# Performance work log

Measured on AMD Instinct MI355X. Metric: run time of the kernel, lower is better.

## Reference

```python
import jax, jax.numpy as jnp
import numpy as np

# ROIAlign config (torchvision semantics, aligned=False)
SPATIAL_SCALE = 0.25
POOLED = 7
SAMPLING_RATIO = 2
MODE = "max"  # from __init__ mode='max'


def setup_inputs() -> dict:
    key = jax.random.key(0)
    kf, kcx, kcy, kw, kh, kb = jax.random.split(key, 6)
    B, C, H, W = 2, 256, 200, 304
    N = 512
    IMG_H, IMG_W = H / SPATIAL_SCALE, W / SPATIAL_SCALE
    feature = jax.random.normal(kf, (B, C, H, W), dtype=jnp.float32)
    cx = jax.random.uniform(kcx, (N,)) * IMG_W
    cy = jax.random.uniform(kcy, (N,)) * IMG_H
    bw = jax.random.uniform(kw, (N,)) * 192.0 + 16.0
    bh = jax.random.uniform(kh, (N,)) * 192.0 + 16.0
    x1 = jnp.clip(cx - bw * 0.5, 0.0, IMG_W - 2.0)
    y1 = jnp.clip(cy - bh * 0.5, 0.0, IMG_H - 2.0)
    x2 = jnp.clip(cx + bw * 0.5, x1 + 1.0, IMG_W - 1.0)
    y2 = jnp.clip(cy + bh * 0.5, y1 + 1.0, IMG_H - 1.0)
    boxes = jnp.stack([x1, y1, x2, y2], axis=1).astype(jnp.float32)
    batch_idx = jax.random.randint(kb, (N,), 0, B, dtype=jnp.int32)
    return {"feature": feature, "boxes": boxes, "batch_idx": batch_idx}


def _sample_coords(start, size):
    # start,size: [N]; returns [N, POOLED*SAMPLING_RATIO] sample coordinates
    bin_sz = size / POOLED                         # [N]
    p = jnp.arange(POOLED, dtype=jnp.float32)      # bin index
    s = (jnp.arange(SAMPLING_RATIO, dtype=jnp.float32) + 0.5) / SAMPLING_RATIO
    # coord = start + (p + s) * bin_sz  -> [N, POOLED, RATIO]
    c = start[:, None, None] + (p[None, :, None] + s[None, None, :]) * bin_sz[:, None, None]
    return c.reshape(c.shape[0], POOLED * SAMPLING_RATIO)


def roi_align(feature, boxes, batch_idx):
    B, C, H, W = feature.shape
    roi = boxes * SPATIAL_SCALE                    # [N,4] in feature coords
    rs_x, rs_y, re_x, re_y = roi[:, 0], roi[:, 1], roi[:, 2], roi[:, 3]
    roi_w = jnp.maximum(re_x - rs_x, 1.0)
    roi_h = jnp.maximum(re_y - rs_y, 1.0)
    ys = _sample_coords(rs_y, roi_h)               # [N, Sy]
    xs = _sample_coords(rs_x, roi_w)               # [N, Sx]
    y = jnp.broadcast_to(ys[:, :, None], (ys.shape[0], ys.shape[1], xs.shape[1]))
    x = jnp.broadcast_to(xs[:, None, :], y.shape)  # [N, Sy, Sx]

    valid = (y > -1.0) & (y < H) & (x > -1.0) & (x < W)
    y = jnp.clip(y, 0.0, H - 1)
    x = jnp.clip(x, 0.0, W - 1)
    y0 = jnp.floor(y).astype(jnp.int32)
    x0 = jnp.floor(x).astype(jnp.int32)
    y1 = jnp.minimum(y0 + 1, H - 1)
    x1 = jnp.minimum(x0 + 1, W - 1)
    ly = y - y0.astype(y.dtype)
    lx = x - x0.astype(x.dtype)
    hy, hx = 1.0 - ly, 1.0 - lx
    b = batch_idx[:, None, None]
    # advanced indexing -> [N, Sy, Sx, C]
    val = (hy * hx)[..., None] * feature[b, :, y0, x0] \
        + (hy * lx)[..., None] * feature[b, :, y0, x1] \
        + (ly * hx)[..., None] * feature[b, :, y1, x0] \
        + (ly * lx)[..., None] * feature[b, :, y1, x1]
    val = jnp.where(valid[..., None], val, 0.0)
    N = boxes.shape[0]
    val = val.reshape(N, POOLED, SAMPLING_RATIO, POOLED, SAMPLING_RATIO, C)
    if MODE == "max":
        out = val.max(axis=(2, 4))                 # [N, PH, PW, C]
    else:
        out = val.mean(axis=(2, 4))
    return jnp.transpose(out, (0, 3, 1, 2))        # [N, C, PH, PW]


def reference(feature, boxes, batch_idx):
    return roi_align(feature, boxes, batch_idx)
```

## Files before the change

kernel.cpp:

```cpp
#include <hip/hip_runtime.h>


#define SPATIAL_SCALE 0.25f
#define POOLED 7
#define SR 2

constexpr int Cc = 256;
constexpr int Hc = 200;
constexpr int Wc = 304;
constexpr int Nc = 512;

constexpr int CG      = 4;
constexpr int TILES   = Cc / CG;
constexpr int NSAMP   = POOLED * SR;
constexpr int NROW    = NSAMP * 2;
constexpr int GRP     = 264;
constexpr int CH_F    = 7 * GRP;
constexpr int BUF_F   = CG * CH_F;
constexpr int CELLS   = POOLED * POOLED;
constexpr int PER_BOX = Cc * CELLS;
constexpr int PLANE   = Hc * Wc;

__global__ __launch_bounds__(256) void roi_align_max_kernel(
    const float* __restrict__ feature,
    const float* __restrict__ boxes,
    const int*   __restrict__ batch_idx,
    float*       __restrict__ out)
{
    __shared__ float lds[2 * BUF_F];

    const int n   = blockIdx.x;
    const int tid = threadIdx.x;
    const int wv     = tid >> 6;
    const int lane   = tid & 63;
    const int lane16 = lane & 15;
    const int rquad  = lane >> 4;

    const float rsx = boxes[n * 4 + 0] * SPATIAL_SCALE;
    const float rsy = boxes[n * 4 + 1] * SPATIAL_SCALE;
    const float rex = boxes[n * 4 + 2] * SPATIAL_SCALE;
    const float rey = boxes[n * 4 + 3] * SPATIAL_SCALE;
    const float roi_w = fmaxf(rex - rsx, 1.0f);
    const float roi_h = fmaxf(rey - rsy, 1.0f);
    const float bin_w = roi_w / (float)POOLED;
    const float bin_h = roi_h / (float)POOLED;
    const int   b     = batch_idx[n];

    const float x_first = __fadd_rn(rsx, __fmul_rn(0.25f, bin_w));
    const float xc0     = fminf(fmaxf(x_first, 0.0f), (float)(Wc - 1));
    const int   xbase   = ((int)floorf(xc0)) & ~3;

    const float x_last = __fadd_rn(rsx, __fmul_rn(6.75f, bin_w));
    const float xlc    = fminf(fmaxf(x_last, 0.0f), (float)(Wc - 1));
    const int   x0l    = (int)floorf(xlc);
    const int   xlastc = min(x0l + 1, Wc - 1);
    const int   span   = xlastc - xbase + 1;
    const int   nl4    = (span + 4) >> 2;

    int ro[7];
    #pragma unroll
    for (int it = 0; it < 7; ++it) {
        const int  slot  = it * 4 + rquad;
        const int  which = slot >= NSAMP;
        const int  sY    = which ? slot - NSAMP : slot;
        const float py   = fmaf((float)sY, 0.5f, 0.25f);
        const float fy   = __fadd_rn(rsy, __fmul_rn(py, bin_h));
        const float fyc  = fminf(fmaxf(fy, 0.0f), (float)(Hc - 1));
        const int   y0   = (int)floorf(fyc);
        const int   row  = which ? min(y0 + 1, Hc - 1) : y0;
        ro[it] = row * Wc;
    }
    const int  col = min(xbase + lane16 * 4, Wc - 4);
    const bool act = (lane16 < nl4);

    const int cell = min(lane, CELLS - 1);
    const int ph   = cell / POOLED;
    const int pw   = cell - ph * POOLED;

    float w00[2][2], w01[2][2], w10[2][2], w11[2][2];
    int   r0a[2][2], r1a[2][2];
    #pragma unroll
    for (int sy = 0; sy < SR; ++sy) {
        const int   sY  = ph * SR + sy;
        const float py  = (float)ph + ((float)sy + 0.5f) * 0.5f;
        const float fy  = __fadd_rn(rsy, __fmul_rn(py, bin_h));
        const bool  vy  = (fy > -1.0f) && (fy < (float)Hc);
        const float fyc = fminf(fmaxf(fy, 0.0f), (float)(Hc - 1));
        const int   y0i = (int)floorf(fyc);
        const float ly  = fyc - (float)y0i;
        const float hy  = 1.0f - ly;
        #pragma unroll
        for (int sx = 0; sx < SR; ++sx) {
            const float px  = (float)pw + ((float)sx + 0.5f) * 0.5f;
            const float fx  = __fadd_rn(rsx, __fmul_rn(px, bin_w));
            const bool  vx  = (fx > -1.0f) && (fx < (float)Wc);
            const float fxc = fminf(fmaxf(fx, 0.0f), (float)(Wc - 1));
            const int   x0i = (int)floorf(fxc);
            const float lx  = fxc - (float)x0i;
            const float hx  = 1.0f - lx;
            const int   c0  = x0i - xbase;
            const bool  v   = vy && vx;
            w00[sy][sx] = v ? hy * hx : 0.0f;
            w01[sy][sx] = v ? hy * lx : 0.0f;
            w10[sy][sx] = v ? ly * hx : 0.0f;
            w11[sy][sx] = v ? ly * lx : 0.0f;
            const int s0 = sY;
            const int s1 = NSAMP + sY;
            r0a[sy][sx] = (s0 >> 2) * GRP + (s0 & 3) * 64 + c0;
            r1a[sy][sx] = (s1 >> 2) * GRP + (s1 & 3) * 64 + c0;
        }
    }

    const float* __restrict__ gp0 =
        feature + ((size_t)b * Cc + wv) * (size_t)PLANE;

#define ISSUE_TILE(GT, Q)                                                     \
    if (act) {                                                                \
        _Pragma("unroll")                                                     \
        for (int it = 0; it < 7; ++it) {                                      \
            const float* gsrc = (GT) + ro[it] + col;                          \
            const int lofs = __builtin_amdgcn_readfirstlane(                  \
                ((Q) * BUF_F + wv * CH_F + it * GRP) * 4);                    \
            __builtin_amdgcn_global_load_lds(                                 \
                (const __attribute__((address_space(1))) unsigned int*)       \
                    (const void*)gsrc,                                        \
                (__attribute__((address_space(3))) unsigned int*)             \
                    (void*)((char*)lds + lofs),                               \
                16, 0, 0);                                                    \
        }                                                                     \
    }

    ISSUE_TILE(gp0, 0)
    const float* __restrict__ gnext = gp0 + (size_t)CG * PLANE;

    for (int j = 0; j < TILES; ++j) {
        if (j + 1 < TILES) {
            ISSUE_TILE(gnext, ((j + 1) & 1))
            gnext += (size_t)CG * PLANE;
            asm volatile("s_waitcnt vmcnt(7)" ::: "memory");
        } else {
            asm volatile("s_waitcnt vmcnt(0)" ::: "memory");
        }

        const int qb = (j & 1) * BUF_F + wv * CH_F;
        float m = -INFINITY;
        #pragma unroll
        for (int sy = 0; sy < SR; ++sy) {
            #pragma unroll
            for (int sx = 0; sx < SR; ++sx) {
                const int a0 = qb + r0a[sy][sx];
                const int a1 = qb + r1a[sy][sx];
                const float bil = w00[sy][sx] * lds[a0]
                                + w01[sy][sx] * lds[a0 + 1]
                                + w10[sy][sx] * lds[a1]
                                + w11[sy][sx] * lds[a1 + 1];
                m = fmaxf(m, bil);
            }
        }
        if (lane < CELLS)
            out[(size_t)n * PER_BOX + (size_t)(j * CG + wv) * CELLS + cell] = m;
    }
#undef ISSUE_TILE
}

extern "C" void kernel_launch(void* const* d_in, const int* in_sizes, int n_in,
                              void* d_out, int out_size, void* d_ws, size_t ws_size,
                              hipStream_t stream) {
    const float* feature   = (const float*)d_in[0];
    const float* boxes     = (const float*)d_in[1];
    const int*   batch_idx = (const int*)d_in[2];
    float*       out       = (float*)d_out;

    roi_align_max_kernel<<<Nc, 256, 0, stream>>>(feature, boxes,
                                                 batch_idx, out);
}
```

Baseline: 227.1 us.

## Sort boxes by batch and vertical band to improve per-XCD cache locality

Adds a small ranking kernel that sorts boxes by (batch index, vertical band of box center) and writes a permutation into the workspace. The main kernel maps block IDs through that permutation, and the (bid&7)*64+(bid>>3) mapping places boxes that are spatially close on the same XCD, so they share feature rows in that XCD's L2. The cost is an extra kernel launch and an extra indirect load per block. It also depends on a workspace being supplied.

```diff
diff --git a/kernel.cpp b/kernel.cpp
--- a/kernel.cpp
+++ b/kernel.cpp
@@ -21,15 +21,45 @@
 constexpr int PER_BOX = Cc * CELLS;
 constexpr int PLANE   = Hc * Wc;
 
+__global__ __launch_bounds__(64) void box_rank_kernel(
+    const float* __restrict__ boxes,
+    const int*   __restrict__ batch_idx,
+    int*         __restrict__ perm)
+{
+    const int n = blockIdx.x;
+    const int l = threadIdx.x;
+
+    const float cyn  = (boxes[n * 4 + 1] + boxes[n * 4 + 3])
+                     * (0.5f * SPATIAL_SCALE);
+    const int  bandn = min(3, max(0, (int)(cyn * (4.0f / (float)Hc))));
+    const int  keyn  = batch_idx[n] * 4 + bandn;
+
+    int rank = 0;
+    #pragma unroll
+    for (int m = 0; m < Nc / 64; ++m) {
+        const int j = m * 64 + l;
+        const float cyj  = (boxes[j * 4 + 1] + boxes[j * 4 + 3])
+                         * (0.5f * SPATIAL_SCALE);
+        const int  bandj = min(3, max(0, (int)(cyj * (4.0f / (float)Hc))));
+        const int  keyj  = batch_idx[j] * 4 + bandj;
+        const bool lt = (keyj < keyn) || (keyj == keyn && j < n);
+        rank += (int)__popcll(__ballot(lt));
+    }
+    if (l == 0) perm[rank] = n;
+}
+
+template <bool USE_PERM>
 __global__ __launch_bounds__(256) void roi_align_max_kernel(
     const float* __restrict__ feature,
     const float* __restrict__ boxes,
     const int*   __restrict__ batch_idx,
+    const int*   __restrict__ perm,
     float*       __restrict__ out)
 {
     __shared__ float lds[2 * BUF_F];
 
-    const int n   = blockIdx.x;
+    const int bid = blockIdx.x;
+    const int n = USE_PERM ? perm[(bid & 7) * 64 + (bid >> 3)] : bid;
     const int tid = threadIdx.x;
     const int wv     = tid >> 6;
     const int lane   = tid & 63;
@@ -171,6 +201,13 @@
     const int*   batch_idx = (const int*)d_in[2];
     float*       out       = (float*)d_out;
 
-    roi_align_max_kernel<<<Nc, 256, 0, stream>>>(feature, boxes,
-                                                 batch_idx, out);
+    if (d_ws != nullptr && ws_size >= (size_t)Nc * sizeof(int)) {
+        int* perm = (int*)d_ws;
+        box_rank_kernel<<<Nc, 64, 0, stream>>>(boxes, batch_idx, perm);
+        roi_align_max_kernel<true><<<Nc, 256, 0, stream>>>(
+            feature, boxes, batch_idx, perm, out);
+    } else {
+        roi_align_max_kernel<false><<<Nc, 256, 0, stream>>>(
+            feature, boxes, batch_idx, nullptr, out);
+    }
 }
```

Result: no change. 223.5 us (-1.5%).

## Stream feature planes per channel through an LDS row ring with sorted boxes

Applied to the files above, without the earlier changes.

Adds a prep kernel that sorts boxes by batch and top row and precomputes per-sample row and column interpolation tables into workspace. The main kernel is restructured so each block owns one (batch, channel) plane and streams its rows through a 64-row LDS ring. Groups of up to five boxes that fit in the window are processed together, so each feature row is read once per channel instead of once per box. This trades redundant global reads for an extra launch, serial box grouping and more barriers, and keeps the old per-box kernel as a fallback when workspace is missing.

```diff
diff --git a/kernel.cpp b/kernel.cpp
--- a/kernel.cpp
+++ b/kernel.cpp
@@ -1,166 +1,327 @@
 #include <hip/hip_runtime.h>
 
 
-#define SPATIAL_SCALE 0.25f
+#define SS 0.25f
 #define POOLED 7
-#define SR 2
 
 constexpr int Cc = 256;
 constexpr int Hc = 200;
 constexpr int Wc = 304;
 constexpr int Nc = 512;
 
-constexpr int CG      = 4;
-constexpr int TILES   = Cc / CG;
-constexpr int NSAMP   = POOLED * SR;
-constexpr int NROW    = NSAMP * 2;
-constexpr int GRP     = 264;
-constexpr int CH_F    = 7 * GRP;
-constexpr int BUF_F   = CG * CH_F;
-constexpr int CELLS   = POOLED * POOLED;
+constexpr int CELLS   = 49;
 constexpr int PER_BOX = Cc * CELLS;
 constexpr int PLANE   = Hc * Wc;
-
-__global__ __launch_bounds__(256) void roi_align_max_kernel(
-    const float* __restrict__ feature,
+constexpr int PLANE_B = PLANE * 4;
+constexpr int RING_ROWS = 64;
+constexpr int WIN     = 63;
+constexpr int RING_F  = RING_ROWS * Wc;
+constexpr int RING_B  = RING_F * 4;
+constexpr int RING_CH = RING_B / 1024;
+constexpr int G   = 5;
+constexpr int NS  = 14;
+
+constexpr int    TBL_OFF_B     = 2048;
+constexpr int    TBL_STRIDE_I4 = 28;
+constexpr size_t WS_NEED = TBL_OFF_B + (size_t)Nc * TBL_STRIDE_I4 * 16;
+
+__global__ __launch_bounds__(64) void roi_prep_kernel(
     const float* __restrict__ boxes,
     const int*   __restrict__ batch_idx,
+    unsigned int* __restrict__ meta,
+    int4*        __restrict__ tbl)
+{
+    const int n = blockIdx.x, l = threadIdx.x;
+
+    const float rsx = boxes[n*4+0]*SS, rsy = boxes[n*4+1]*SS;
+    const float rex = boxes[n*4+2]*SS, rey = boxes[n*4+3]*SS;
+    const float bin_h = fmaxf(rey - rsy, 1.0f) / (float)POOLED;
+    const float bin_w = fmaxf(rex - rsx, 1.0f) / (float)POOLED;
+    const int   batch = batch_idx[n];
+
+    const float fy0 = __fadd_rn(rsy, __fmul_rn(0.25f, bin_h));
+    const int y0min = (int)floorf(fminf(fmaxf(fy0, 0.f), (float)(Hc-1)));
+    const float fyL = __fadd_rn(rsy, __fmul_rn(6.75f, bin_h));
+    const int   yL  = (int)floorf(fminf(fmaxf(fyL, 0.f), (float)(Hc-1)));
+    const int ymax  = min(yL + 1, Hc - 1);
+    const unsigned key = (unsigned)(batch * 256 + y0min);
+
+    int rank = 0;
+    #pragma unroll
+    for (int m = 0; m < Nc/64; ++m) {
+        const int j = m*64 + l;
+        const float rsyj = boxes[j*4+1]*SS, reyj = boxes[j*4+3]*SS;
+        const float bhj  = fmaxf(reyj - rsyj, 1.0f) / (float)POOLED;
+        const float fyj  = __fadd_rn(rsyj, __fmul_rn(0.25f, bhj));
+        const int   yj   = (int)floorf(fminf(fmaxf(fyj,0.f),(float)(Hc-1)));
+        const unsigned keyj = (unsigned)(batch_idx[j]*256 + yj);
+        const bool lt = (keyj < key) || (keyj == key && j < n);
+        rank += (int)__popcll(__ballot(lt));
+    }
+    if (l == 0)
+        meta[rank] = (unsigned)n | ((unsigned)batch << 9)
+                   | ((unsigned)y0min << 10) | ((unsigned)ymax << 18);
+
+    if (l < NS) {
+        const float py  = fmaf((float)l, 0.5f, 0.25f);
+        const float fy  = __fadd_rn(rsy, __fmul_rn(py, bin_h));
+        const bool  vy  = (fy > -1.0f) && (fy < (float)Hc);
+        const float fyc = fminf(fmaxf(fy, 0.f), (float)(Hc-1));
+        const int   y0  = (int)floorf(fyc);
+        const float ly  = fyc - (float)y0, hy = 1.0f - ly;
+        int4 r; r.x = y0;
+        r.y = __float_as_int(vy ? hy : 0.0f);
+        r.z = __float_as_int(vy ? ly : 0.0f); r.w = 0;
+        tbl[n*TBL_STRIDE_I4 + l] = r;
+    } else if (l >= 16 && l < 16 + NS) {
+        const int s = l - 16;
+        const float px  = fmaf((float)s, 0.5f, 0.25f);
+        const float fx  = __fadd_rn(rsx, __fmul_rn(px, bin_w));
+        const bool  vx  = (fx > -1.0f) && (fx < (float)Wc);
+        const float fxc = fminf(fmaxf(fx, 0.f), (float)(Wc-1));
+        const int   x0  = (int)floorf(fxc);
+        const float lx  = fxc - (float)x0, hx = 1.0f - lx;
+        int4 r; r.x = x0;
+        r.y = __float_as_int(vx ? hx : 0.0f);
+        r.z = __float_as_int(vx ? lx : 0.0f); r.w = 0;
+        tbl[n*TBL_STRIDE_I4 + NS + s] = r;
+    }
+}
+
+__global__ __launch_bounds__(256) void roi_stream_kernel(
+    const float* __restrict__ feature,
+    const unsigned int* __restrict__ meta,
+    const int4*  __restrict__ tbl,
     float*       __restrict__ out)
 {
-    __shared__ float lds[2 * BUF_F];
-
-    const int n   = blockIdx.x;
-    const int tid = threadIdx.x;
-    const int wv     = tid >> 6;
-    const int lane   = tid & 63;
-    const int lane16 = lane & 15;
-    const int rquad  = lane >> 4;
-
-    const float rsx = boxes[n * 4 + 0] * SPATIAL_SCALE;
-    const float rsy = boxes[n * 4 + 1] * SPATIAL_SCALE;
-    const float rex = boxes[n * 4 + 2] * SPATIAL_SCALE;
-    const float rey = boxes[n * 4 + 3] * SPATIAL_SCALE;
-    const float roi_w = fmaxf(rex - rsx, 1.0f);
-    const float roi_h = fmaxf(rey - rsy, 1.0f);
-    const float bin_w = roi_w / (float)POOLED;
-    const float bin_h = roi_h / (float)POOLED;
-    const int   b     = batch_idx[n];
-
-    const float x_first = __fadd_rn(rsx, __fmul_rn(0.25f, bin_w));
-    const float xc0     = fminf(fmaxf(x_first, 0.0f), (float)(Wc - 1));
-    const int   xbase   = ((int)floorf(xc0)) & ~3;
-
-    const float x_last = __fadd_rn(rsx, __fmul_rn(6.75f, bin_w));
-    const float xlc    = fminf(fmaxf(x_last, 0.0f), (float)(Wc - 1));
-    const int   x0l    = (int)floorf(xlc);
-    const int   xlastc = min(x0l + 1, Wc - 1);
-    const int   span   = xlastc - xbase + 1;
-    const int   nl4    = (span + 4) >> 2;
+    __shared__ float ring[RING_F];
+
+    const int bid = blockIdx.x;
+    const int X = bid & 7, b = (bid >> 3) & 1, cj = bid >> 4;
+    const int c = X * 32 + cj;
+    const char* __restrict__ plane =
+        (const char*)(feature + ((size_t)b * Cc + c) * (size_t)PLANE);
+
+    const int tid = threadIdx.x, wv = tid >> 6, lane = tid & 63;
+    const int bg   = tid / CELLS;
+    const int cell = tid - bg * CELLS;
+    const int ph   = cell / POOLED, pw = cell - ph * POOLED;
+    const bool hasCell = (tid < G * CELLS);
+
+    int p = 0, loadedT = 0;
+
+    int cntA=0, yfA=0, tmA=0, nA0=0,nA1=0,nA2=0,nA3=0,nA4=0;
+    int cntB=0, yfB=0, tmB=0, nB0=0,nB1=0,nB2=0,nB3=0,nB4=0;
+    int4 ya0, ya1, xa0, xa1, yb0, yb1, xb0, xb1;
+
+#define COLLECT(CNT,YF,TM,N0,N1,N2,N3,N4) {                                  \
+    CNT = 0; YF = 0; TM = 0;                                                 \
+    while (p < Nc) {                                                         \
+        const unsigned mm = meta[p];                                         \
+        const int bt = (int)((mm >> 9) & 1u);                                \
+        if (bt != b) { if (bt < b) { ++p; continue; } else break; }          \
+        const int ymin = (int)((mm >> 10) & 255u);                           \
+        const int ymx  = (int)((mm >> 18) & 255u);                           \
+        const int nn   = (int)(mm & 511u);                                   \
+        if (CNT == 0) { YF = ymin; N0 = N1 = N2 = N3 = N4 = nn; }            \
+        else if (ymx + 1 > YF + WIN) break;                                  \
+        if      (CNT == 1) N1 = nn; else if (CNT == 2) N2 = nn;              \
+        else if (CNT == 3) N3 = nn; else if (CNT == 4) N4 = nn;              \
+        TM = max(TM, ymx + 1);                                               \
+        ++CNT; ++p;                                                          \
+        if (CNT == G) break;                                                 \
+    }                                                                        \
+}
+
+#define ISSUE(FROMT, TOT) {                                                  \
+    const int kc0 = (19*(FROMT) + 15) >> 4, kc1 = (19*(TOT) + 15) >> 4;      \
+    for (int k = kc0 + ((wv - kc0) & 3); k < kc1; k += 4) {                  \
+        const int km  = k % RING_CH;                                         \
+        const int off = k * 1024 + lane * 16;                                \
+        if (off < PLANE_B) {                                                 \
+            const int ldst = __builtin_amdgcn_readfirstlane(km * 1024);      \
+            __builtin_amdgcn_global_load_lds(                                \
+                (const __attribute__((address_space(1))) unsigned int*)      \
+                    (const void*)(plane + off),                              \
+                (__attribute__((address_space(3))) unsigned int*)            \
+                    (void*)((char*)ring + ldst), 16, 0, 0);                  \
+        }                                                                    \
+    }                                                                        \
+}
+
+#define LOADREC(N0,N1,N2,N3,N4, Y0,Y1,X0,X1) {                               \
+    const int nSel = (bg==0)?(N0):(bg==1)?(N1):(bg==2)?(N2):(bg==3)?(N3):(N4);\
+    const int4* tb = tbl + (size_t)nSel * TBL_STRIDE_I4;                     \
+    Y0 = tb[ph*2 + 0]; Y1 = tb[ph*2 + 1];                                    \
+    X0 = tb[NS + pw*2 + 0]; X1 = tb[NS + pw*2 + 1];                          \
+}
+
+#define COMPUTE(CNT,N0,N1,N2,N3,N4, Y0,Y1,X0,X1) {                           \
+    float mres = -INFINITY;                                                  \
+    _Pragma("unroll")                                                        \
+    for (int sy = 0; sy < 2; ++sy) {                                         \
+        const int4 yr = sy ? (Y1) : (Y0);                                    \
+        const int   yy = yr.x;                                               \
+        const float hy = __int_as_float(yr.y), ly = __int_as_float(yr.z);    \
+        const int ra = (yy & 63) * Wc;                                       \
+        const int rb = (min(yy + 1, Hc - 1) & 63) * Wc;                      \
+        _Pragma("unroll")                                                    \
+        for (int sx = 0; sx < 2; ++sx) {                                     \
+            const int4 xr = sx ? (X1) : (X0);                                \
+            const int   xx = xr.x;                                           \
+            const float hx = __int_as_float(xr.y), lx = __int_as_float(xr.z);\
+            const int cb = min(xx + 1, Wc - 1);                              \
+            const float v00 = ring[ra + xx], v01 = ring[ra + cb];            \
+            const float v10 = ring[rb + xx], v11 = ring[rb + cb];            \
+            const float s = hy*hx*v00 + hy*lx*v01 + ly*hx*v10 + ly*lx*v11;   \
+            mres = fmaxf(mres, s);                                           \
+        }                                                                    \
+    }                                                                        \
+    if (hasCell && bg < (CNT)) {                                             \
+        const int nS = (bg==0)?(N0):(bg==1)?(N1):(bg==2)?(N2):(bg==3)?(N3):(N4);\
+        out[(size_t)nS * PER_BOX + (size_t)c * CELLS + cell] = mres;         \
+    }                                                                        \
+}
+
+    COLLECT(cntA, yfA, tmA, nA0, nA1, nA2, nA3, nA4);
+    if (cntA == 0) return;
+    {
+        const int tgt = min(yfA + WIN, Hc);
+        ISSUE(0, tgt); loadedT = tgt;
+    }
+    LOADREC(nA0, nA1, nA2, nA3, nA4, ya0, ya1, xa0, xa1);
+    __syncthreads();
+
+    while (cntA) {
+        COLLECT(cntB, yfB, tmB, nB0, nB1, nB2, nB3, nB4);
+        if (cntB) {
+            const int tgt = min(yfA + WIN, Hc);
+            if (tgt > loadedT) { ISSUE(loadedT, tgt); loadedT = tgt; }
+            LOADREC(nB0, nB1, nB2, nB3, nB4, yb0, yb1, xb0, xb1);
+        }
+        COMPUTE(cntA, nA0, nA1, nA2, nA3, nA4, ya0, ya1, xa0, xa1);
+        __syncthreads();
+        if (cntB && tmB > loadedT) {
+            ISSUE(loadedT, tmB); loadedT = tmB;
+            __syncthreads();
+        }
+        cntA = cntB; yfA = yfB; tmA = tmB;
+        nA0 = nB0; nA1 = nB1; nA2 = nB2; nA3 = nB3; nA4 = nB4;
+        ya0 = yb0; ya1 = yb1; xa0 = xb0; xa1 = xb1;
+    }
+
+#undef COLLECT
+#undef ISSUE
+#undef LOADREC
+#undef COMPUTE
+}
+
+constexpr int FCG = 4, FTILES = Cc/FCG, FNSAMP = 14;
+constexpr int FGRP = 264, FCH_F = 7*FGRP, FBUF_F = FCG*FCH_F;
+
+__global__ __launch_bounds__(256) void roi_fallback_kernel(
+    const float* __restrict__ feature, const float* __restrict__ boxes,
+    const int* __restrict__ batch_idx, float* __restrict__ out)
+{
+    __shared__ float lds[2*FBUF_F];
+    const int n = blockIdx.x, tid = threadIdx.x;
+    const int wvv = tid >> 6, lane = tid & 63;
+    const int lane16 = lane & 15, rquad = lane >> 4;
+
+    const float rsx = boxes[n*4+0]*SS, rsy = boxes[n*4+1]*SS;
+    const float rex = boxes[n*4+2]*SS, rey = boxes[n*4+3]*SS;
+    const float bin_w = fmaxf(rex-rsx,1.f)/7.f, bin_h = fmaxf(rey-rsy,1.f)/7.f;
+    const int b = batch_idx[n];
+    const float xc0 = fminf(fmaxf(__fadd_rn(rsx,__fmul_rn(0.25f,bin_w)),0.f),(float)(Wc-1));
+    const int xbase = ((int)floorf(xc0)) & ~3;
+    const float xlc = fminf(fmaxf(__fadd_rn(rsx,__fmul_rn(6.75f,bin_w)),0.f),(float)(Wc-1));
+    const int span = min((int)floorf(xlc)+1, Wc-1) - xbase + 1;
+    const int nl4 = (span + 4) >> 2;
 
     int ro[7];
     #pragma unroll
     for (int it = 0; it < 7; ++it) {
-        const int  slot  = it * 4 + rquad;
-        const int  which = slot >= NSAMP;
-        const int  sY    = which ? slot - NSAMP : slot;
-        const float py   = fmaf((float)sY, 0.5f, 0.25f);
-        const float fy   = __fadd_rn(rsy, __fmul_rn(py, bin_h));
-        const float fyc  = fminf(fmaxf(fy, 0.0f), (float)(Hc - 1));
-        const int   y0   = (int)floorf(fyc);
-        const int   row  = which ? min(y0 + 1, Hc - 1) : y0;
-        ro[it] = row * Wc;
-    }
-    const int  col = min(xbase + lane16 * 4, Wc - 4);
+        const int slot = it*4 + rquad;
+        const int which = slot >= FNSAMP;
+        const int sY = which ? slot - FNSAMP : slot;
+        const float fy = __fadd_rn(rsy, __fmul_rn(fmaf((float)sY,0.5f,0.25f), bin_h));
+        const float fyc = fminf(fmaxf(fy,0.f),(float)(Hc-1));
+        const int y0 = (int)floorf(fyc);
+        ro[it] = (which ? min(y0+1,Hc-1) : y0) * Wc;
+    }
+    const int col = min(xbase + lane16*4, Wc-4);
     const bool act = (lane16 < nl4);
-
-    const int cell = min(lane, CELLS - 1);
-    const int ph   = cell / POOLED;
-    const int pw   = cell - ph * POOLED;
+    const int cell = min(lane, CELLS-1);
+    const int ph = cell/POOLED, pw = cell - ph*POOLED;
 
     float w00[2][2], w01[2][2], w10[2][2], w11[2][2];
-    int   r0a[2][2], r1a[2][2];
+    int r0a[2][2], r1a[2][2];
     #pragma unroll
-    for (int sy = 0; sy < SR; ++sy) {
-        const int   sY  = ph * SR + sy;
-        const float py  = (float)ph + ((float)sy + 0.5f) * 0.5f;
-        const float fy  = __fadd_rn(rsy, __fmul_rn(py, bin_h));
-        const bool  vy  = (fy > -1.0f) && (fy < (float)Hc);
-        const float fyc = fminf(fmaxf(fy, 0.0f), (float)(Hc - 1));
-        const int   y0i = (int)floorf(fyc);
-        const float ly  = fyc - (float)y0i;
-        const float hy  = 1.0f - ly;
+    for (int sy = 0; sy < 2; ++sy) {
+        const int sY = ph*2+sy;
+        const float fy = __fadd_rn(rsy, __fmul_rn((float)ph + ((float)sy+0.5f)*0.5f, bin_h));
+        const bool vy = (fy>-1.f)&&(fy<(float)Hc);
+        const float fyc = fminf(fmaxf(fy,0.f),(float)(Hc-1));
+        const int y0i = (int)floorf(fyc);
+        const float ly = fyc-(float)y0i, hy = 1.f-ly;
         #pragma unroll
-        for (int sx = 0; sx < SR; ++sx) {
-            const float px  = (float)pw + ((float)sx + 0.5f) * 0.5f;
-            const float fx  = __fadd_rn(rsx, __fmul_rn(px, bin_w));
-            const bool  vx  = (fx > -1.0f) && (fx < (float)Wc);
-            const float fxc = fminf(fmaxf(fx, 0.0f), (float)(Wc - 1));
-            const int   x0i = (int)floorf(fxc);
-            const float lx  = fxc - (float)x0i;
-            const float hx  = 1.0f - lx;
-            const int   c0  = x0i - xbase;
-            const bool  v   = vy && vx;
-            w00[sy][sx] = v ? hy * hx : 0.0f;
-            w01[sy][sx] = v ? hy * lx : 0.0f;
-            w10[sy][sx] = v ? ly * hx : 0.0f;
-            w11[sy][sx] = v ? ly * lx : 0.0f;
-            const int s0 = sY;
-            const int s1 = NSAMP + sY;
-            r0a[sy][sx] = (s0 >> 2) * GRP + (s0 & 3) * 64 + c0;
-            r1a[sy][sx] = (s1 >> 2) * GRP + (s1 & 3) * 64 + c0;
+        for (int sx = 0; sx < 2; ++sx) {
+            const float fx = __fadd_rn(rsx, __fmul_rn((float)pw + ((float)sx+0.5f)*0.5f, bin_w));
+            const bool vx = (fx>-1.f)&&(fx<(float)Wc);
+            const float fxc = fminf(fmaxf(fx,0.f),(float)(Wc-1));
+            const int x0i = (int)floorf(fxc);
+            const float lx = fxc-(float)x0i, hx = 1.f-lx;
+            const int c0 = x0i - xbase;
+            const bool v = vy && vx;
+            w00[sy][sx] = v ? hy*hx : 0.f; w01[sy][sx] = v ? hy*lx : 0.f;
+            w10[sy][sx] = v ? ly*hx : 0.f; w11[sy][sx] = v ? ly*lx : 0.f;
+            r0a[sy][sx] = (sY>>2)*FGRP + (sY&3)*64 + c0;
+            const int s1 = FNSAMP + sY;
+            r1a[sy][sx] = (s1>>2)*FGRP + (s1&3)*64 + c0;
         }
     }
-
-    const float* __restrict__ gp0 =
-        feature + ((size_t)b * Cc + wv) * (size_t)PLANE;
-
-#define ISSUE_TILE(GT, Q)                                                     \
+    const float* __restrict__ gp0 = feature + ((size_t)b*Cc + wvv)*(size_t)PLANE;
+
+#define FISSUE(GT, Q)                                                         \
     if (act) {                                                                \
         _Pragma("unroll")                                                     \
         for (int it = 0; it < 7; ++it) {                                      \
             const float* gsrc = (GT) + ro[it] + col;                          \
             const int lofs = __builtin_amdgcn_readfirstlane(                  \
-                ((Q) * BUF_F + wv * CH_F + it * GRP) * 4);                    \
+                ((Q)*FBUF_F + wvv*FCH_F + it*FGRP)*4);                        \
             __builtin_amdgcn_global_load_lds(                                 \
                 (const __attribute__((address_space(1))) unsigned int*)       \
                     (const void*)gsrc,                                        \
                 (__attribute__((address_space(3))) unsigned int*)             \
-                    (void*)((char*)lds + lofs),                               \
-                16, 0, 0);                                                    \
+                    (void*)((char*)lds + lofs), 16, 0, 0);                    \
         }                                                                     \
     }
 
-    ISSUE_TILE(gp0, 0)
-    const float* __restrict__ gnext = gp0 + (size_t)CG * PLANE;
-
-    for (int j = 0; j < TILES; ++j) {
-        if (j + 1 < TILES) {
-            ISSUE_TILE(gnext, ((j + 1) & 1))
-            gnext += (size_t)CG * PLANE;
+    FISSUE(gp0, 0)
+    const float* __restrict__ gnext = gp0 + (size_t)FCG*PLANE;
+    for (int j = 0; j < FTILES; ++j) {
+        if (j + 1 < FTILES) {
+            FISSUE(gnext, ((j+1)&1))
+            gnext += (size_t)FCG*PLANE;
             asm volatile("s_waitcnt vmcnt(7)" ::: "memory");
         } else {
             asm volatile("s_waitcnt vmcnt(0)" ::: "memory");
         }
-
-        const int qb = (j & 1) * BUF_F + wv * CH_F;
+        const int qb = (j&1)*FBUF_F + wvv*FCH_F;
         float m = -INFINITY;
         #pragma unroll
-        for (int sy = 0; sy < SR; ++sy) {
+        for (int sy = 0; sy < 2; ++sy)
             #pragma unroll
-            for (int sx = 0; sx < SR; ++sx) {
-                const int a0 = qb + r0a[sy][sx];
-                const int a1 = qb + r1a[sy][sx];
-                const float bil = w00[sy][sx] * lds[a0]
-                                + w01[sy][sx] * lds[a0 + 1]
-                                + w10[sy][sx] * lds[a1]
-                                + w11[sy][sx] * lds[a1 + 1];
+            for (int sx = 0; sx < 2; ++sx) {
+                const int a0 = qb + r0a[sy][sx], a1 = qb + r1a[sy][sx];
+                const float bil = w00[sy][sx]*lds[a0] + w01[sy][sx]*lds[a0+1]
+                                + w10[sy][sx]*lds[a1] + w11[sy][sx]*lds[a1+1];
                 m = fmaxf(m, bil);
             }
-        }
         if (lane < CELLS)
-            out[(size_t)n * PER_BOX + (size_t)(j * CG + wv) * CELLS + cell] = m;
-    }
-#undef ISSUE_TILE
+            out[(size_t)n*PER_BOX + (size_t)(j*FCG + wvv)*CELLS + cell] = m;
+    }
+#undef FISSUE
 }
 
 extern "C" void kernel_launch(void* const* d_in, const int* in_sizes, int n_in,
@@ -171,6 +332,13 @@
     const int*   batch_idx = (const int*)d_in[2];
     float*       out       = (float*)d_out;
 
-    roi_align_max_kernel<<<Nc, 256, 0, stream>>>(feature, boxes,
-                                                 batch_idx, out);
-}
+    if (d_ws != nullptr && ws_size >= WS_NEED) {
+        unsigned int* meta = (unsigned int*)d_ws;
+        int4* tbl = (int4*)((char*)d_ws + TBL_OFF_B);
+        roi_prep_kernel<<<Nc, 64, 0, stream>>>(boxes, batch_idx, meta, tbl);
+        roi_stream_kernel<<<Nc, 256, 0, stream>>>(feature, meta, tbl, out);
+    } else {
+        roi_fallback_kernel<<<Nc, 256, 0, stream>>>(feature, boxes,
+                                                    batch_idx, out);
+    }
+}
```

Result: slower. 280.3 us (+23.5%).
